# Performance work log

Hardware: AMD Instinct MI355X
Metric: run time of the kernel (lower is better)

## Reference

```python
import jax, jax.numpy as jnp
import numpy as np

D_MODEL = 512
NUM_HEADS = 8
HEAD_DIM = D_MODEL // NUM_HEADS


def setup_inputs() -> dict:
    key = jax.random.key(0)
    ks = jax.random.split(key, 9)
    B, N, D = 2, 4096, D_MODEL
    scale = 1.0 / np.sqrt(D)
    inp = {
        "x": jax.random.normal(ks[0], (B, N, D), dtype=jnp.float32),
        "wq": jax.random.normal(ks[1], (D, D), dtype=jnp.float32) * scale,
        "bq": jnp.zeros((D,), dtype=jnp.float32),
        "wk": jax.random.normal(ks[2], (D, D), dtype=jnp.float32) * scale,
        "bk": jnp.zeros((D,), dtype=jnp.float32),
        "wv": jax.random.normal(ks[3], (D, D), dtype=jnp.float32) * scale,
        "bv": jnp.zeros((D,), dtype=jnp.float32),
        "wo": jax.random.normal(ks[4], (D, D), dtype=jnp.float32) * scale,
        "bo": jnp.zeros((D,), dtype=jnp.float32),
    }
    return inp


def reference(x, wq, bq, wk, bk, wv, bv, wo, bo):
    B, N, D = x.shape
    h, dh = NUM_HEADS, HEAD_DIM
    # QKV projections (torch Linear: x @ W.T + b); reshape to [B, h, N, dh]
    def proj(w, b):
        y = jnp.einsum('bnd,ed->bne', x, w) + b
        return y.reshape(B, N, h, dh).transpose(0, 2, 1, 3)
    q = proj(wq, bq)
    k = proj(wk, bk)
    v = proj(wv, bv)
    # scaled dot-product attention, full [B, h, N, N] scores (matches module)
    attn = jnp.einsum('bhqd,bhkd->bhqk', q, k) / jnp.sqrt(jnp.float32(dh)).astype(x.dtype)
    attn = jax.nn.softmax(attn, axis=-1)
    y = jnp.einsum('bhqk,bhkd->bhqd', attn, v)
    y = y.transpose(0, 2, 1, 3).reshape(B, N, D)
    # output projection
    return jnp.einsum('bnd,ed->bne', y, wo) + bo
```

## Files before the change

kernel.cpp:

```cpp
#include <hip/hip_runtime.h>
#include <hip/hip_bf16.h>

#define NN 4096
#define DD 512
#define HH 8
#define DH 64
#define BN 8192
#define PAIRS 16

typedef unsigned int uint32;
typedef __attribute__((ext_vector_type(8))) short short8;
typedef __attribute__((ext_vector_type(4))) float f32x4;

__device__ __forceinline__ unsigned short f2b(float x) {
    union { float f; uint32 u; } c; c.f = x;
    return (unsigned short)((c.u + 0x8000u) >> 16);
}
__device__ __forceinline__ uint32 pack2(float lo, float hi) {
    return (uint32)f2b(lo) | ((uint32)f2b(hi) << 16);
}
__device__ __forceinline__ uint32 cvtpk(float lo, float hi) {
    uint32 r;
    asm("v_cvt_pk_bf16_f32 %0, %1, %2" : "=v"(r) : "v"(lo), "v"(hi));
    return r;
}
__device__ __forceinline__ float expsc(float s) {
    return __builtin_amdgcn_exp2f(s);
}
#define QSCALE 0.18033688011112042f

__device__ __forceinline__ void gload16(const void* g, void* l) {
    __builtin_amdgcn_global_load_lds(
        (const __attribute__((address_space(1))) void*)g,
        (__attribute__((address_space(3))) void*)l, 16, 0, 0);
}

__device__ __forceinline__ uint32 dtype_flag_wave(const uint32* __restrict__ xw) {
    int lane = threadIdx.x & 63;
    int c = 0;
    #pragma unroll
    for (int r = 0; r < 16; ++r) {
        uint32 e = (xw[lane + r * 64] >> 7) & 0xFFu;
        if (e >= 110u && e <= 135u) c++;
    }
    c += __shfl_xor(c, 1);  c += __shfl_xor(c, 2);  c += __shfl_xor(c, 4);
    c += __shfl_xor(c, 8);  c += __shfl_xor(c, 16); c += __shfl_xor(c, 32);
    return (c < 512) ? 1u : 0u;
}

__global__ __launch_bounds__(256) void conv_all(
    const void* __restrict__ xsrc,
    const void* w0, const void* w1, const void* w2, const void* w3,
    const void* b0, const void* b1, const void* b2, const void* b3,
    unsigned short* __restrict__ xb,
    unsigned short* __restrict__ wsb,
    float* __restrict__ bsf)
{
    const uint32 fp32mode = dtype_flag_wave((const uint32*)xsrc);
    const int bid = blockIdx.x;
    if (bid < 2048) {
        int i0 = (bid * 256 + threadIdx.x) * 8;
        if (fp32mode) {
            const float4* s = (const float4*)xsrc;
            float4 a = s[i0 >> 2], b = s[(i0 >> 2) + 1];
            uint4 o;
            o.x = pack2(a.x, a.y); o.y = pack2(a.z, a.w);
            o.z = pack2(b.x, b.y); o.w = pack2(b.z, b.w);
            *(uint4*)(xb + i0) = o;
        } else {
            *(uint4*)(xb + i0) = ((const uint4*)xsrc)[i0 >> 3];
        }
    } else if (bid < 2560) {
        int bb = bid - 2048;
        int seg = bb >> 7;
        const void* src = (seg == 0) ? w0 : (seg == 1) ? w1 : (seg == 2) ? w2 : w3;
        unsigned short* d = wsb + (size_t)seg * DD * DD;
        int i0 = ((bb & 127) * 256 + threadIdx.x) * 8;
        if (fp32mode) {
            const float4* s = (const float4*)src;
            float4 a = s[i0 >> 2], b = s[(i0 >> 2) + 1];
            uint4 o;
            o.x = pack2(a.x, a.y); o.y = pack2(a.z, a.w);
            o.z = pack2(b.x, b.y); o.w = pack2(b.z, b.w);
            *(uint4*)(d + i0) = o;
        } else {
            *(uint4*)(d + i0) = ((const uint4*)src)[i0 >> 3];
        }
    } else {
        const void* sl[4] = { b0, b1, b2, b3 };
        #pragma unroll
        for (int m = 0; m < 4; ++m) {
            #pragma unroll
            for (int j = 0; j < 2; ++j) {
                int i = threadIdx.x * 2 + j;
                float v;
                if (fp32mode) v = ((const float*)sl[m])[i];
                else {
                    union { uint32 u; float f; } c;
                    c.u = ((uint32)((const unsigned short*)sl[m])[i]) << 16;
                    v = c.f;
                }
                bsf[m * DD + i] = v;
            }
        }
    }
}

__global__ __launch_bounds__(256) void qkv_gemm(
    const unsigned short* __restrict__ xb,
    const unsigned short* __restrict__ wsb,
    const float* __restrict__ bsf,
    unsigned short* __restrict__ Qb, unsigned short* __restrict__ Kb,
    unsigned short* __restrict__ VTg)
{
    __shared__ unsigned short As[128 * 32];
    __shared__ unsigned short Bs[128 * 32];
    const int tid = threadIdx.x;
    const int mat = blockIdx.x >> 8;
    const int rem = blockIdx.x & 255;
    const int nt = rem >> 6, mt = rem & 63;
    const int m0 = mt * 128, n0 = nt * 128;
    const int w = tid >> 6, lane = tid & 63, quad = lane >> 4, col = lane & 15;
    const int wr = w >> 1, wc = w & 1;
    const unsigned short* wm = wsb + (size_t)mat * DD * DD;
    const bool qk = (mat < 2);

    f32x4 acc[4][4];
    #pragma unroll
    for (int i = 0; i < 4; ++i)
        #pragma unroll
        for (int j = 0; j < 4; ++j)
            acc[i][j] = (f32x4){0.f, 0.f, 0.f, 0.f};

    for (int kt = 0; kt < 16; ++kt) {
        int k0 = kt * 32;
        __syncthreads();
        #pragma unroll
        for (int it = 0; it < 2; ++it) {
            int idx = tid + it * 256;
            int row = idx >> 2, c4 = idx & 3;
            unsigned short* lA = &As[(size_t)(it * 256 + w * 64) * 8];
            unsigned short* lB = &Bs[(size_t)(it * 256 + w * 64) * 8];
            gload16(xb + (size_t)(m0 + row) * DD + k0 + c4 * 8, lA);
            gload16(wm + (size_t)(n0 + row) * DD + k0 + c4 * 8, lB);
        }
        __syncthreads();
        if (qk) {
            short8 wf[4], xf[4];
            #pragma unroll
            for (int i = 0; i < 4; ++i)
                wf[i] = *(const short8*)&Bs[(wr * 64 + i * 16 + col) * 32 + quad * 8];
            #pragma unroll
            for (int j = 0; j < 4; ++j)
                xf[j] = *(const short8*)&As[(wc * 64 + j * 16 + col) * 32 + quad * 8];
            #pragma unroll
            for (int i = 0; i < 4; ++i)
                #pragma unroll
                for (int j = 0; j < 4; ++j)
                    acc[i][j] = __builtin_amdgcn_mfma_f32_16x16x32_bf16(
                        wf[i], xf[j], acc[i][j], 0, 0, 0);
        } else {
            short8 xf[4], wf[4];
            #pragma unroll
            for (int i = 0; i < 4; ++i)
                xf[i] = *(const short8*)&As[(wr * 64 + i * 16 + col) * 32 + quad * 8];
            #pragma unroll
            for (int j = 0; j < 4; ++j)
                wf[j] = *(const short8*)&Bs[(wc * 64 + j * 16 + col) * 32 + quad * 8];
            #pragma unroll
            for (int i = 0; i < 4; ++i)
                #pragma unroll
                for (int j = 0; j < 4; ++j)
                    acc[i][j] = __builtin_amdgcn_mfma_f32_16x16x32_bf16(
                        xf[i], wf[j], acc[i][j], 0, 0, 0);
        }
    }

    if (qk) {
        unsigned short* Om = (mat == 0) ? Qb : Kb;
        const float qs = (mat == 0) ? QSCALE : 1.0f;
        #pragma unroll
        for (int i = 0; i < 4; ++i) {
            int e0 = n0 + wr * 64 + i * 16 + quad * 4;
            float4 bj = *(const float4*)(bsf + mat * DD + e0);
            int h = e0 >> 6, jj0 = e0 & 63;
            #pragma unroll
            for (int j = 0; j < 4; ++j) {
                int g = m0 + wc * 64 + j * 16 + col;
                int b = g >> 12, n = g & (NN - 1);
                uint32 lo = pack2((acc[i][j][0] + bj.x) * qs, (acc[i][j][1] + bj.y) * qs);
                uint32 hi = pack2((acc[i][j][2] + bj.z) * qs, (acc[i][j][3] + bj.w) * qs);
                uint2 v; v.x = lo; v.y = hi;
                *(uint2*)(Om + ((size_t)((b << 3) + h) * NN + n) * DH + jj0) = v;
            }
        }
    } else {
        #pragma unroll
        for (int j = 0; j < 4; ++j) {
            int e = n0 + wc * 64 + j * 16 + col;
            float bj = bsf[2 * DD + e];
            int h = e >> 6, jj = e & 63;
            #pragma unroll
            for (int i = 0; i < 4; ++i) {
                int g0 = m0 + wr * 64 + i * 16 + quad * 4;
                int b = g0 >> 12, n = g0 & (NN - 1);
                uint32 lo = pack2(acc[i][j][0] + bj, acc[i][j][1] + bj);
                uint32 hi = pack2(acc[i][j][2] + bj, acc[i][j][3] + bj);
                uint2 v; v.x = lo; v.y = hi;
                *(uint2*)(VTg + ((size_t)((b << 3) + h) * DH + jj) * NN + n) = v;
            }
        }
    }
}

__global__ __launch_bounds__(512, 4) void attn_mfma(
    const unsigned short* __restrict__ Qb,
    const unsigned short* __restrict__ Kb,
    const unsigned short* __restrict__ VTg,
    unsigned short* __restrict__ Ob)
{
    __shared__ unsigned short Kt[2][64 * 72];
    __shared__ unsigned short Vt[2][64 * 72];

    const int tid  = threadIdx.x;
    const int w    = tid >> 6;
    const int lane = tid & 63;
    const int quad = lane >> 4;
    const int col  = lane & 15;
    const int pair = blockIdx.x >> 5;
    const int chunk = blockIdx.x & 31;
    const size_t base = (size_t)pair * NN;
    const int n0 = chunk * 128;
    const int qbase = w * 16;

    short8 qf[2];
    #pragma unroll
    for (int kk = 0; kk < 2; ++kk)
        qf[kk] = *(const short8*)(Qb +
            (base + n0 + qbase + col) * DH + kk * 32 + quad * 8);

    f32x4 accO[4];
    #pragma unroll
    for (int tc = 0; tc < 4; ++tc) accO[tc] = (f32x4){0.f, 0.f, 0.f, 0.f};
    float lsum = 0.f;

    const int skey = tid >> 3;
    const int sc8  = (tid & 7) * 8;
    const unsigned short* Kg = Kb + base * DH;
    const unsigned short* Vg = VTg + (size_t)pair * DH * NN;

    uint4 kreg = *(const uint4*)(Kg + (size_t)skey * DH + sc8);
    uint4 vreg = *(const uint4*)(Vg + (size_t)skey * NN + sc8);
    *(uint4*)&Kt[0][skey * 72 + sc8] = kreg;
    *(uint4*)&Vt[0][skey * 72 + sc8] = vreg;
    kreg = *(const uint4*)(Kg + (size_t)(64 + skey) * DH + sc8);
    vreg = *(const uint4*)(Vg + (size_t)skey * NN + 64 + sc8);
    __syncthreads();

    for (int kt = 0; kt < NN / 64; ++kt) {
        const int buf = kt & 1;
        if (kt + 1 < NN / 64) {
            *(uint4*)&Kt[buf ^ 1][skey * 72 + sc8] = kreg;
            *(uint4*)&Vt[buf ^ 1][skey * 72 + sc8] = vreg;
            int tn = (kt + 2 < NN / 64) ? kt + 2 : 0;
            kreg = *(const uint4*)(Kg + (size_t)(tn * 64 + skey) * DH + sc8);
            vreg = *(const uint4*)(Vg + (size_t)skey * NN + tn * 64 + sc8);
        }
        const unsigned short* Kc = &Kt[buf][0];
        const unsigned short* Vc = &Vt[buf][0];

        short8 pf[2];
        #pragma unroll
        for (int half = 0; half < 2; ++half) {
            f32x4 s0 = (f32x4){0.f, 0.f, 0.f, 0.f};
            f32x4 s1 = (f32x4){0.f, 0.f, 0.f, 0.f};
            __builtin_amdgcn_s_setprio(1);
            #pragma unroll
            for (int kk = 0; kk < 2; ++kk) {
                short8 kf0 = *(const short8*)&Kc[((half * 2 + 0) * 16 + col) * 72 + kk * 32 + quad * 8];
                short8 kf1 = *(const short8*)&Kc[((half * 2 + 1) * 16 + col) * 72 + kk * 32 + quad * 8];
                s0 = __builtin_amdgcn_mfma_f32_16x16x32_bf16(kf0, qf[kk], s0, 0, 0, 0);
                s1 = __builtin_amdgcn_mfma_f32_16x16x32_bf16(kf1, qf[kk], s1, 0, 0, 0);
            }
            __builtin_amdgcn_s_setprio(0);

            float p00 = expsc(s0[0]), p01 = expsc(s0[1]);
            float p02 = expsc(s0[2]), p03 = expsc(s0[3]);
            float p10 = expsc(s1[0]), p11 = expsc(s1[1]);
            float p12 = expsc(s1[2]), p13 = expsc(s1[3]);
            lsum += ((p00 + p01) + (p02 + p03)) + ((p10 + p11) + (p12 + p13));
            uint32 a0 = cvtpk(p00, p01);
            uint32 a1 = cvtpk(p02, p03);
            uint32 b0 = cvtpk(p10, p11);
            uint32 b1 = cvtpk(p12, p13);
            asm("v_permlane32_swap_b32 %0, %1" : "+v"(a0), "+v"(b0));
            asm("v_permlane32_swap_b32 %0, %1" : "+v"(a1), "+v"(b1));
            asm("v_permlane16_swap_b32 %0, %1" : "+v"(a0), "+v"(b0));
            asm("v_permlane16_swap_b32 %0, %1" : "+v"(a1), "+v"(b1));
            union { uint32 u[4]; short8 v; } pu;
            pu.u[0] = a0; pu.u[1] = a1; pu.u[2] = b0; pu.u[3] = b1;
            pf[half] = pu.v;
        }

        __builtin_amdgcn_s_setprio(1);
        #pragma unroll
        for (int tc = 0; tc < 4; ++tc) {
            short8 vf0 = *(const short8*)&Vc[(tc * 16 + col) * 72 + quad * 8];
            short8 vf1 = *(const short8*)&Vc[(tc * 16 + col) * 72 + 32 + quad * 8];
            accO[tc] = __builtin_amdgcn_mfma_f32_16x16x32_bf16(pf[0], vf0, accO[tc], 0, 0, 0);
            accO[tc] = __builtin_amdgcn_mfma_f32_16x16x32_bf16(pf[1], vf1, accO[tc], 0, 0, 0);
        }
        __builtin_amdgcn_s_setprio(0);

        __syncthreads();
    }

    lsum += __shfl_xor(lsum, 16);
    lsum += __shfl_xor(lsum, 32);

    float inv[4];
    #pragma unroll
    for (int r = 0; r < 4; ++r)
        inv[r] = 1.f / __shfl(lsum, quad * 4 + r);

    #pragma unroll
    for (int tc = 0; tc < 4; ++tc)
        #pragma unroll
        for (int r = 0; r < 4; ++r) {
            float v = accO[tc][r] * inv[r];
            Ob[(base + n0 + qbase + quad * 4 + r) * DH + tc * 16 + col] = f2b(v);
        }
}

__global__ __launch_bounds__(256) void out_gemm(
    const unsigned short* __restrict__ Ob,
    const unsigned short* __restrict__ wob,
    const float* __restrict__ bof,
    const void* __restrict__ xsrc,
    void* __restrict__ outp)
{
    __shared__ unsigned short As[128 * 32];
    __shared__ unsigned short Bs[128 * 32];
    const int tid = threadIdx.x;
    const int nt = blockIdx.x >> 6, mt = blockIdx.x & 63;
    const int m0 = mt * 128, n0 = nt * 128;
    const int w = tid >> 6, lane = tid & 63, quad = lane >> 4, col = lane & 15;
    const int wr = w >> 1, wc = w & 1;
    const int fp32mode = (int)dtype_flag_wave((const uint32*)xsrc);

    f32x4 acc[4][4];
    #pragma unroll
    for (int i = 0; i < 4; ++i)
        #pragma unroll
        for (int j = 0; j < 4; ++j)
            acc[i][j] = (f32x4){0.f, 0.f, 0.f, 0.f};

    for (int kt = 0; kt < 16; ++kt) {
        int k0 = kt * 32;
        int h = k0 >> 6, koff = k0 & 63;
        __syncthreads();
        #pragma unroll
        for (int it = 0; it < 2; ++it) {
            int idx = tid + it * 256;
            int row = idx >> 2, c4 = idx & 3;
            int g = m0 + row, b = g >> 12, n = g & (NN - 1);
            unsigned short* lA = &As[(size_t)(it * 256 + w * 64) * 8];
            unsigned short* lB = &Bs[(size_t)(it * 256 + w * 64) * 8];
            gload16(Ob + ((size_t)((b << 3) + h) * NN + n) * DH + koff + c4 * 8, lA);
            gload16(wob + (size_t)(n0 + row) * DD + k0 + c4 * 8, lB);
        }
        __syncthreads();
        short8 wf[4], yf[4];
        #pragma unroll
        for (int i = 0; i < 4; ++i)
            wf[i] = *(const short8*)&Bs[(wr * 64 + i * 16 + col) * 32 + quad * 8];
        #pragma unroll
        for (int j = 0; j < 4; ++j)
            yf[j] = *(const short8*)&As[(wc * 64 + j * 16 + col) * 32 + quad * 8];
        #pragma unroll
        for (int i = 0; i < 4; ++i)
            #pragma unroll
            for (int j = 0; j < 4; ++j)
                acc[i][j] = __builtin_amdgcn_mfma_f32_16x16x32_bf16(
                    wf[i], yf[j], acc[i][j], 0, 0, 0);
    }

    #pragma unroll
    for (int i = 0; i < 4; ++i) {
        int e0 = n0 + wr * 64 + i * 16 + quad * 4;
        float4 bj = *(const float4*)(bof + e0);
        #pragma unroll
        for (int j = 0; j < 4; ++j) {
            int g = m0 + wc * 64 + j * 16 + col;
            float v0 = acc[i][j][0] + bj.x;
            float v1 = acc[i][j][1] + bj.y;
            float v2 = acc[i][j][2] + bj.z;
            float v3 = acc[i][j][3] + bj.w;
            if (fp32mode) {
                float4 o; o.x = v0; o.y = v1; o.z = v2; o.w = v3;
                *(float4*)((float*)outp + (size_t)g * DD + e0) = o;
            } else {
                uint2 o; o.x = pack2(v0, v1); o.y = pack2(v2, v3);
                *(uint2*)((unsigned short*)outp + (size_t)g * DD + e0) = o;
            }
        }
    }
}

extern "C" void kernel_launch(void* const* d_in, const int* in_sizes, int n_in,
                              void* d_out, int out_size, void* d_ws, size_t ws_size,
                              hipStream_t stream) {
    char* p = (char*)d_ws;
    unsigned short* xb  = (unsigned short*)p;   p += (size_t)BN * DD * 2;
    unsigned short* wsb = (unsigned short*)p;   p += (size_t)4 * DD * DD * 2;
    float*          bsf = (float*)p;            p += (size_t)4 * DD * 4;
    unsigned short* Qb  = (unsigned short*)p;   p += (size_t)PAIRS * NN * DH * 2;
    unsigned short* Kb  = (unsigned short*)p;   p += (size_t)PAIRS * NN * DH * 2;
    unsigned short* VTg = (unsigned short*)p;   p += (size_t)PAIRS * NN * DH * 2;
    unsigned short* Ob  = (unsigned short*)p;   p += (size_t)PAIRS * NN * DH * 2;

    conv_all<<<2561, 256, 0, stream>>>(d_in[0],
                                       d_in[1], d_in[3], d_in[5], d_in[7],
                                       d_in[2], d_in[4], d_in[6], d_in[8],
                                       xb, wsb, bsf);
    qkv_gemm<<<768, 256, 0, stream>>>(xb, wsb, bsf, Qb, Kb, VTg);
    attn_mfma<<<PAIRS * 32, 512, 0, stream>>>(Qb, Kb, VTg, Ob);
    out_gemm<<<256, 256, 0, stream>>>(Ob, wsb + (size_t)3 * DD * DD,
                                      bsf + 3 * DD, d_in[0], d_out);
}
```

Measured before the change: 216.4 us.

## Process two query subtiles per wave in attention to reuse K/V fragments

Each wave in the attention kernel now handles 32 query rows (two 16-row subtiles) instead of 16, and blocks shrink from 512 to 256 threads. K and V fragments read from LDS are reused across both subtiles, which halves the LDS reads per MFMA. Each thread now stages two 16-byte chunks of K and V per tile. The cost is higher register pressure (double the accumulators and P fragments) and fewer waves per block, which cuts the latency hiding available from other waves.

```diff
diff --git a/kernel.cpp b/kernel.cpp
--- a/kernel.cpp
+++ b/kernel.cpp
@@ -213,7 +213,7 @@
     }
 }
 
-__global__ __launch_bounds__(512, 4) void attn_mfma(
+__global__ __launch_bounds__(256, 2) void attn_mfma(
     const unsigned short* __restrict__ Qb,
     const unsigned short* __restrict__ Kb,
     const unsigned short* __restrict__ VTg,
@@ -231,104 +231,142 @@
     const int chunk = blockIdx.x & 31;
     const size_t base = (size_t)pair * NN;
     const int n0 = chunk * 128;
-    const int qbase = w * 16;
-
-    short8 qf[2];
-    #pragma unroll
-    for (int kk = 0; kk < 2; ++kk)
-        qf[kk] = *(const short8*)(Qb +
-            (base + n0 + qbase + col) * DH + kk * 32 + quad * 8);
-
-    f32x4 accO[4];
-    #pragma unroll
-    for (int tc = 0; tc < 4; ++tc) accO[tc] = (f32x4){0.f, 0.f, 0.f, 0.f};
-    float lsum = 0.f;
-
-    const int skey = tid >> 3;
-    const int sc8  = (tid & 7) * 8;
+    const int qbase = w * 32;
+
+    short8 qf[2][2];
+    #pragma unroll
+    for (int qs = 0; qs < 2; ++qs)
+        #pragma unroll
+        for (int kk = 0; kk < 2; ++kk)
+            qf[qs][kk] = *(const short8*)(Qb +
+                (base + n0 + qbase + qs * 16 + col) * DH + kk * 32 + quad * 8);
+
+    f32x4 accO[2][4];
+    #pragma unroll
+    for (int qs = 0; qs < 2; ++qs)
+        #pragma unroll
+        for (int tc = 0; tc < 4; ++tc)
+            accO[qs][tc] = (f32x4){0.f, 0.f, 0.f, 0.f};
+    float lsum0 = 0.f, lsum1 = 0.f;
+
+    const int srow = tid >> 2;
+    const int sce  = (tid & 3) * 16;
     const unsigned short* Kg = Kb + base * DH;
     const unsigned short* Vg = VTg + (size_t)pair * DH * NN;
 
-    uint4 kreg = *(const uint4*)(Kg + (size_t)skey * DH + sc8);
-    uint4 vreg = *(const uint4*)(Vg + (size_t)skey * NN + sc8);
-    *(uint4*)&Kt[0][skey * 72 + sc8] = kreg;
-    *(uint4*)&Vt[0][skey * 72 + sc8] = vreg;
-    kreg = *(const uint4*)(Kg + (size_t)(64 + skey) * DH + sc8);
-    vreg = *(const uint4*)(Vg + (size_t)skey * NN + 64 + sc8);
+    uint4 kreg[2], vreg[2];
+    #pragma unroll
+    for (int r = 0; r < 2; ++r) {
+        kreg[r] = *(const uint4*)(Kg + (size_t)srow * DH + sce + r * 8);
+        vreg[r] = *(const uint4*)(Vg + (size_t)srow * NN + sce + r * 8);
+    }
+    #pragma unroll
+    for (int r = 0; r < 2; ++r) {
+        *(uint4*)&Kt[0][srow * 72 + sce + r * 8] = kreg[r];
+        *(uint4*)&Vt[0][srow * 72 + sce + r * 8] = vreg[r];
+    }
+    #pragma unroll
+    for (int r = 0; r < 2; ++r) {
+        kreg[r] = *(const uint4*)(Kg + (size_t)(64 + srow) * DH + sce + r * 8);
+        vreg[r] = *(const uint4*)(Vg + (size_t)srow * NN + 64 + sce + r * 8);
+    }
     __syncthreads();
 
     for (int kt = 0; kt < NN / 64; ++kt) {
         const int buf = kt & 1;
         if (kt + 1 < NN / 64) {
-            *(uint4*)&Kt[buf ^ 1][skey * 72 + sc8] = kreg;
-            *(uint4*)&Vt[buf ^ 1][skey * 72 + sc8] = vreg;
+            #pragma unroll
+            for (int r = 0; r < 2; ++r) {
+                *(uint4*)&Kt[buf ^ 1][srow * 72 + sce + r * 8] = kreg[r];
+                *(uint4*)&Vt[buf ^ 1][srow * 72 + sce + r * 8] = vreg[r];
+            }
             int tn = (kt + 2 < NN / 64) ? kt + 2 : 0;
-            kreg = *(const uint4*)(Kg + (size_t)(tn * 64 + skey) * DH + sc8);
-            vreg = *(const uint4*)(Vg + (size_t)skey * NN + tn * 64 + sc8);
+            #pragma unroll
+            for (int r = 0; r < 2; ++r) {
+                kreg[r] = *(const uint4*)(Kg + (size_t)(tn * 64 + srow) * DH + sce + r * 8);
+                vreg[r] = *(const uint4*)(Vg + (size_t)srow * NN + tn * 64 + sce + r * 8);
+            }
         }
         const unsigned short* Kc = &Kt[buf][0];
         const unsigned short* Vc = &Vt[buf][0];
 
-        short8 pf[2];
+        short8 pf[2][2];
         #pragma unroll
         for (int half = 0; half < 2; ++half) {
-            f32x4 s0 = (f32x4){0.f, 0.f, 0.f, 0.f};
-            f32x4 s1 = (f32x4){0.f, 0.f, 0.f, 0.f};
-            __builtin_amdgcn_s_setprio(1);
-            #pragma unroll
-            for (int kk = 0; kk < 2; ++kk) {
-                short8 kf0 = *(const short8*)&Kc[((half * 2 + 0) * 16 + col) * 72 + kk * 32 + quad * 8];
-                short8 kf1 = *(const short8*)&Kc[((half * 2 + 1) * 16 + col) * 72 + kk * 32 + quad * 8];
-                s0 = __builtin_amdgcn_mfma_f32_16x16x32_bf16(kf0, qf[kk], s0, 0, 0, 0);
-                s1 = __builtin_amdgcn_mfma_f32_16x16x32_bf16(kf1, qf[kk], s1, 0, 0, 0);
-            }
-            __builtin_amdgcn_s_setprio(0);
-
-            float p00 = expsc(s0[0]), p01 = expsc(s0[1]);
-            float p02 = expsc(s0[2]), p03 = expsc(s0[3]);
-            float p10 = expsc(s1[0]), p11 = expsc(s1[1]);
-            float p12 = expsc(s1[2]), p13 = expsc(s1[3]);
-            lsum += ((p00 + p01) + (p02 + p03)) + ((p10 + p11) + (p12 + p13));
-            uint32 a0 = cvtpk(p00, p01);
-            uint32 a1 = cvtpk(p02, p03);
-            uint32 b0 = cvtpk(p10, p11);
-            uint32 b1 = cvtpk(p12, p13);
-            asm("v_permlane32_swap_b32 %0, %1" : "+v"(a0), "+v"(b0));
-            asm("v_permlane32_swap_b32 %0, %1" : "+v"(a1), "+v"(b1));
-            asm("v_permlane16_swap_b32 %0, %1" : "+v"(a0), "+v"(b0));
-            asm("v_permlane16_swap_b32 %0, %1" : "+v"(a1), "+v"(b1));
-            union { uint32 u[4]; short8 v; } pu;
-            pu.u[0] = a0; pu.u[1] = a1; pu.u[2] = b0; pu.u[3] = b1;
-            pf[half] = pu.v;
-        }
-
-        __builtin_amdgcn_s_setprio(1);
+            short8 kf[2][2];
+            #pragma unroll
+            for (int t = 0; t < 2; ++t)
+                #pragma unroll
+                for (int kk = 0; kk < 2; ++kk)
+                    kf[t][kk] = *(const short8*)&Kc[((half * 2 + t) * 16 + col) * 72 + kk * 32 + quad * 8];
+            #pragma unroll
+            for (int qs = 0; qs < 2; ++qs) {
+                f32x4 s0 = (f32x4){0.f, 0.f, 0.f, 0.f};
+                f32x4 s1 = (f32x4){0.f, 0.f, 0.f, 0.f};
+                __builtin_amdgcn_s_setprio(1);
+                #pragma unroll
+                for (int kk = 0; kk < 2; ++kk) {
+                    s0 = __builtin_amdgcn_mfma_f32_16x16x32_bf16(kf[0][kk], qf[qs][kk], s0, 0, 0, 0);
+                    s1 = __builtin_amdgcn_mfma_f32_16x16x32_bf16(kf[1][kk], qf[qs][kk], s1, 0, 0, 0);
+                }
+                __builtin_amdgcn_s_setprio(0);
+
+                float p00 = expsc(s0[0]), p01 = expsc(s0[1]);
+                float p02 = expsc(s0[2]), p03 = expsc(s0[3]);
+                float p10 = expsc(s1[0]), p11 = expsc(s1[1]);
+                float p12 = expsc(s1[2]), p13 = expsc(s1[3]);
+                float psum = ((p00 + p01) + (p02 + p03)) + ((p10 + p11) + (p12 + p13));
+                if (qs == 0) lsum0 += psum; else lsum1 += psum;
+                uint32 a0 = cvtpk(p00, p01);
+                uint32 a1 = cvtpk(p02, p03);
+                uint32 b0 = cvtpk(p10, p11);
+                uint32 b1 = cvtpk(p12, p13);
+                asm("v_permlane32_swap_b32 %0, %1" : "+v"(a0), "+v"(b0));
+                asm("v_permlane32_swap_b32 %0, %1" : "+v"(a1), "+v"(b1));
+                asm("v_permlane16_swap_b32 %0, %1" : "+v"(a0), "+v"(b0));
+                asm("v_permlane16_swap_b32 %0, %1" : "+v"(a1), "+v"(b1));
+                union { uint32 u[4]; short8 v; } pu;
+                pu.u[0] = a0; pu.u[1] = a1; pu.u[2] = b0; pu.u[3] = b1;
+                pf[qs][half] = pu.v;
+            }
+        }
+
         #pragma unroll
         for (int tc = 0; tc < 4; ++tc) {
             short8 vf0 = *(const short8*)&Vc[(tc * 16 + col) * 72 + quad * 8];
             short8 vf1 = *(const short8*)&Vc[(tc * 16 + col) * 72 + 32 + quad * 8];
-            accO[tc] = __builtin_amdgcn_mfma_f32_16x16x32_bf16(pf[0], vf0, accO[tc], 0, 0, 0);
-            accO[tc] = __builtin_amdgcn_mfma_f32_16x16x32_bf16(pf[1], vf1, accO[tc], 0, 0, 0);
-        }
-        __builtin_amdgcn_s_setprio(0);
+            __builtin_amdgcn_s_setprio(1);
+            #pragma unroll
+            for (int qs = 0; qs < 2; ++qs) {
+                accO[qs][tc] = __builtin_amdgcn_mfma_f32_16x16x32_bf16(pf[qs][0], vf0, accO[qs][tc], 0, 0, 0);
+                accO[qs][tc] = __builtin_amdgcn_mfma_f32_16x16x32_bf16(pf[qs][1], vf1, accO[qs][tc], 0, 0, 0);
+            }
+            __builtin_amdgcn_s_setprio(0);
+        }
 
         __syncthreads();
     }
 
-    lsum += __shfl_xor(lsum, 16);
-    lsum += __shfl_xor(lsum, 32);
-
-    float inv[4];
-    #pragma unroll
-    for (int r = 0; r < 4; ++r)
-        inv[r] = 1.f / __shfl(lsum, quad * 4 + r);
+    lsum0 += __shfl_xor(lsum0, 16);
+    lsum0 += __shfl_xor(lsum0, 32);
+    lsum1 += __shfl_xor(lsum1, 16);
+    lsum1 += __shfl_xor(lsum1, 32);
+
+    float inv0[4], inv1[4];
+    #pragma unroll
+    for (int r = 0; r < 4; ++r) {
+        inv0[r] = 1.f / __shfl(lsum0, quad * 4 + r);
+        inv1[r] = 1.f / __shfl(lsum1, quad * 4 + r);
+    }
 
     #pragma unroll
     for (int tc = 0; tc < 4; ++tc)
         #pragma unroll
         for (int r = 0; r < 4; ++r) {
-            float v = accO[tc][r] * inv[r];
-            Ob[(base + n0 + qbase + quad * 4 + r) * DH + tc * 16 + col] = f2b(v);
+            float v0 = accO[0][tc][r] * inv0[r];
+            float v1 = accO[1][tc][r] * inv1[r];
+            Ob[(base + n0 + qbase + quad * 4 + r) * DH + tc * 16 + col] = f2b(v0);
+            Ob[(base + n0 + qbase + 16 + quad * 4 + r) * DH + tc * 16 + col] = f2b(v1);
         }
 }
 
@@ -424,7 +462,7 @@
                                        d_in[2], d_in[4], d_in[6], d_in[8],
                                        xb, wsb, bsf);
     qkv_gemm<<<768, 256, 0, stream>>>(xb, wsb, bsf, Qb, Kb, VTg);
-    attn_mfma<<<PAIRS * 32, 512, 0, stream>>>(Qb, Kb, VTg, Ob);
+    attn_mfma<<<PAIRS * 32, 256, 0, stream>>>(Qb, Kb, VTg, Ob);
     out_gemm<<<256, 256, 0, stream>>>(Ob, wsb + (size_t)3 * DD * DD,
                                       bsf + 3 * DD, d_in[0], d_out);
 }
```

Measured after the change: 278.0 us. +28.4%, slower.
